# Performance work log

Hardware: AMD Instinct MI355X
Metric: run time of the kernel (lower is better)

Reference implementation:

```python
import jax, jax.numpy as jnp
import numpy as np

N_NODES = 100000
N_EDGES = 1600000
N_GRAPHS = 1000
IN_C = 64
HID = 64
OUT_C = 1
L = 3


def setup_inputs() -> dict:
    key = jax.random.key(0)
    ks = jax.random.split(key, 12)
    x = jax.random.normal(ks[0], (N_NODES, IN_C), dtype=jnp.float32)
    edge_index = jax.random.randint(ks[1], (2, N_EDGES), 0, N_NODES, dtype=jnp.int32)
    batch = jnp.sort(jax.random.randint(ks[2], (N_NODES,), 0, N_GRAPHS, dtype=jnp.int32))
    s = 1.0 / np.sqrt(HID)
    # GraphConv params (all layers 64->64): lin_rel (W,b) applied to aggregated
    # neighbors, lin_root (W, no bias) applied to self features.
    Wrel = jax.random.uniform(ks[3], (L, HID, HID), jnp.float32, -s, s)
    brel = jax.random.uniform(ks[4], (L, HID), jnp.float32, -s, s)
    Wroot = jax.random.uniform(ks[5], (L, HID, HID), jnp.float32, -s, s)
    W1 = jax.random.uniform(ks[6], (HID, 64), jnp.float32, -s, s)
    b1 = jax.random.uniform(ks[7], (64,), jnp.float32, -s, s)
    W2 = jax.random.uniform(ks[8], (64, 32), jnp.float32, -1/8, 1/8)
    b2 = jax.random.uniform(ks[9], (32,), jnp.float32, -1/8, 1/8)
    W3 = jax.random.uniform(ks[10], (32, OUT_C), jnp.float32, -1/np.sqrt(32), 1/np.sqrt(32))
    b3 = jax.random.uniform(ks[11], (OUT_C,), jnp.float32, -1/np.sqrt(32), 1/np.sqrt(32))
    return {"x": x, "edge_index": edge_index, "batch": batch,
            "Wrel": Wrel, "brel": brel, "Wroot": Wroot,
            "W1": W1, "b1": b1, "W2": W2, "b2": b2, "W3": W3, "b3": b3}


def reference(x, edge_index, batch, Wrel, brel, Wroot, W1, b1, W2, b2, W3, b3):
    src, dst = edge_index[0], edge_index[1]
    n = x.shape[0]
    x_add = jnp.zeros((N_GRAPHS, HID), dtype=x.dtype)
    for i in range(L):
        # GraphConv: gather source features, sum-scatter to targets
        agg = jax.ops.segment_sum(x[src], dst, num_segments=n)  # [N, C]
        x = agg @ Wrel[i] + brel[i] + x @ Wroot[i]
        x = jax.nn.relu(x)
        # global_add_pool per layer, accumulated
        x_add = x_add + jax.ops.segment_sum(x, batch, num_segments=N_GRAPHS)
    h = jax.nn.relu(x_add @ W1 + b1)
    h = jax.nn.relu(h @ W2 + b2)
    return h @ W3 + b3  # [N_GRAPHS, OUT_C]
```

## Files before the change

kernel.cpp:

```cpp
#include <hip/hip_runtime.h>
#include <hip/hip_bf16.h>

#define HID 64
#define BN 192
#define MAXB 1024

typedef short  bf16x8 __attribute__((ext_vector_type(8)));
typedef float  f32x4  __attribute__((ext_vector_type(4)));

__device__ inline float bf2f(unsigned int u16) {
    union { unsigned int i; float f; } v; v.i = u16 << 16; return v.f;
}
__device__ inline unsigned short f2bf(float f) {
    union { float f; unsigned int i; } v; v.f = f;
    unsigned int u = v.i;
    u += 0x7FFFu + ((u >> 16) & 1u);
    return (unsigned short)(u >> 16);
}

__global__ __launch_bounds__(1024) void bucket_hist(
        const int* __restrict__ dst, int* __restrict__ cnt,
        int* __restrict__ gHist, int E, int nb) {
    __shared__ int h[MAXB];
    for (int i = threadIdx.x; i < nb; i += 1024) h[i] = 0;
    __syncthreads();
    int base = blockIdx.x * 16384;
    for (int i = 0; i < 16; ++i) {
        int e = base + i * 1024 + threadIdx.x;
        if (e < E) atomicAdd(&h[dst[e] / BN], 1);
    }
    __syncthreads();
    int* gh = gHist + (size_t)blockIdx.x * nb;
    for (int i = threadIdx.x; i < nb; i += 1024) {
        int c = h[i];
        gh[i] = c;
        if (c) atomicAdd(&cnt[i], c);
    }
}

__global__ void bucket_scan(const int* __restrict__ cnt, int* __restrict__ base,
                            int* __restrict__ cursor, int nb, int total) {
    int lane = threadIdx.x;
    int running = 0;
    int nch = (nb + 63) / 64;
    for (int c = 0; c < nch; ++c) {
        int i = c * 64 + lane;
        int v = (i < nb) ? cnt[i] : 0;
        int s = v;
        for (int d = 1; d < 64; d <<= 1) {
            int t = __shfl_up(s, d);
            if (lane >= d) s += t;
        }
        if (i < nb) {
            int ex = running + s - v;
            base[i] = ex;
            cursor[i * 16] = ex;
        }
        running += __shfl(s, 63);
    }
    if (lane == 0) base[nb] = total;
}

__global__ __launch_bounds__(1024) void bucket_scatter(
        const int* __restrict__ src, const int* __restrict__ dst,
        const int* __restrict__ gHist,
        int* __restrict__ cursor, unsigned int* __restrict__ rec, int E, int nb) {
    __shared__ int gb[MAXB];
    __shared__ int lc[MAXB];
    for (int i = threadIdx.x; i < nb; i += 1024) lc[i] = 0;
    const int* gh = gHist + (size_t)blockIdx.x * nb;
    for (int i = threadIdx.x; i < nb; i += 1024) {
        int c = gh[i];
        if (c) gb[i] = atomicAdd(&cursor[i * 16], c);
    }
    __syncthreads();
    int base = blockIdx.x * 16384;
    for (int i = 0; i < 16; ++i) {
        int e = base + i * 1024 + threadIdx.x;
        if (e < E) {
            int d = dst[e];
            int b = d / BN;
            int lp = atomicAdd(&lc[b], 1);
            rec[gb[b] + lp] = ((unsigned int)src[e] << 8) | (unsigned int)(d - b * BN);
        }
    }
}

__global__ __launch_bounds__(256) void bucket_to_csr(
        const unsigned int* __restrict__ rec, const int* __restrict__ bbase,
        int* __restrict__ col, int* __restrict__ rowp, int N, int nb) {
    __shared__ int tmp[256];
    __shared__ int cur[256];
    int b = blockIdx.x;
    int n0 = b * BN;
    int nNodes = min(BN, N - n0);
    int tid = threadIdx.x;
    int e0 = bbase[b], e1 = bbase[b + 1];
    tmp[tid] = 0;
    __syncthreads();
    for (int e = e0 + tid; e < e1; e += 256)
        atomicAdd(&tmp[rec[e] & 255u], 1);
    __syncthreads();
    int my = tmp[tid];
    for (int offd = 1; offd < 256; offd <<= 1) {
        int t = (tid >= offd) ? tmp[tid - offd] : 0;
        __syncthreads();
        tmp[tid] += t;
        __syncthreads();
    }
    int ex = tmp[tid] - my;
    cur[tid] = ex;
    if (tid < nNodes) rowp[n0 + tid] = e0 + ex;
    if (b == nb - 1 && tid == 0) rowp[N] = e1;
    __syncthreads();
    for (int e = e0 + tid; e < e1; e += 256) {
        unsigned int r = rec[e];
        int p = atomicAdd(&cur[r & 255u], 1);
        col[e0 + p] = (int)(r >> 8);
    }
}

__global__ __launch_bounds__(256) void prep_all(
        const float* __restrict__ x0, unsigned int* __restrict__ xb,
        const float* __restrict__ Wrel, const float* __restrict__ Wroot,
        unsigned short* __restrict__ Wt,
        const int* __restrict__ batch, int* __restrict__ bstart,
        int* __restrict__ bcnt, float* __restrict__ x_add,
        int N, int G, int nl, int NB) {
    int i = blockIdx.x * 256 + threadIdx.x;
    if (i < N * 16) {
        float4 v = reinterpret_cast<const float4*>(x0)[i];
        xb[i * 2]     = ((unsigned int)f2bf(v.y) << 16) | f2bf(v.x);
        xb[i * 2 + 1] = ((unsigned int)f2bf(v.w) << 16) | f2bf(v.z);
    }
    if (i < nl * 64 * 128) {
        int k = i & 127, c = (i >> 7) & 63, l = i >> 13;
        float v = (k < 64) ? Wrel[(size_t)l * 4096 + k * 64 + c]
                           : Wroot[(size_t)l * 4096 + (k - 64) * 64 + c];
        Wt[i] = f2bf(v);
    }
    if (i < N) {
        int b = batch[i];
        int prev = (i == 0) ? -1 : batch[i - 1];
        for (int g = prev + 1; g <= b; ++g) bstart[g] = i;
        if (i == N - 1)
            for (int g = b + 1; g <= G; ++g) bstart[g] = N;
    }
    if (i < NB) bcnt[i] = 0;
    if (i < G * 64) x_add[i] = 0.f;
}

__global__ __launch_bounds__(256) void layer_fused(
        const int* __restrict__ rowp, const int* __restrict__ col,
        const unsigned int* __restrict__ xb,
        unsigned short* __restrict__ yout,
        const unsigned short* __restrict__ Wt,
        const float* __restrict__ brel,
        const unsigned int* __restrict__ poolY,
        const int* __restrict__ bstart, float* __restrict__ x_add,
        int n, int nTiles, int G) {
    int tid = threadIdx.x;
    if (blockIdx.x >= nTiles) {
        int g = blockIdx.x - nTiles;
        if (g >= G) return;
        int lane = tid & 63, w = tid >> 6;
        int h = lane >> 5, ch = lane & 31;
        __shared__ float2 part[4][32];
        int s0 = bstart[g], s1 = bstart[g + 1];
        float ax = 0.f, ay = 0.f;
        for (int nd = s0 + w * 2 + h; nd < s1; nd += 8) {
            unsigned int p = poolY[(size_t)nd * 32 + ch];
            ax += bf2f(p & 0xFFFFu);
            ay += bf2f(p >> 16);
        }
        ax += __shfl(ax, lane ^ 32);
        ay += __shfl(ay, lane ^ 32);
        if (h == 0) part[w][ch] = make_float2(ax, ay);
        __syncthreads();
        if (tid < 32) {
            float2 s = part[0][tid];
            s.x += part[1][tid].x + part[2][tid].x + part[3][tid].x;
            s.y += part[1][tid].y + part[2][tid].y + part[3][tid].y;
            float2* xa = reinterpret_cast<float2*>(x_add + (size_t)g * 64);
            float2 cur = xa[tid];
            xa[tid] = make_float2(cur.x + s.x, cur.y + s.y);
        }
        return;
    }

    __shared__ unsigned int aggL[16][36];
    int n0 = blockIdx.x * 16;
    int lane = tid & 63;
    int wv = tid >> 6;
    int half = lane >> 5, ch = lane & 31;

#pragma unroll
    for (int s = 0; s < 2; ++s) {
        int node = n0 + wv * 4 + half * 2 + s;
        if (node < n) {
            int e0 = rowp[node], e1 = rowp[node + 1];
            float ax = 0.f, ay = 0.f;
            for (int eb = e0; eb < e1; eb += 8) {
                int c[8];
#pragma unroll
                for (int j = 0; j < 8; ++j) c[j] = col[min(eb + j, e1 - 1)];
                unsigned int p[8];
#pragma unroll
                for (int j = 0; j < 8; ++j) p[j] = xb[(size_t)c[j] * 32 + ch];
#pragma unroll
                for (int j = 0; j < 8; ++j) {
                    unsigned int q = (eb + j < e1) ? p[j] : 0u;
                    ax += bf2f(q & 0xFFFFu);
                    ay += bf2f(q >> 16);
                }
            }
            aggL[node - n0][ch] = ((unsigned int)f2bf(ay) << 16) | f2bf(ax);
        } else if (node - n0 < 16) {
            aggL[node - n0][ch] = 0u;
        }
    }
    __syncthreads();

    int r = lane & 15, kb = lane >> 4;
    f32x4 acc = {};
    const unsigned short* xrow = reinterpret_cast<const unsigned short*>(xb)
                               + (size_t)min(n0 + r, n - 1) * 64 + kb * 8;
    const unsigned short* wrow = Wt + (size_t)(wv * 16 + r) * 128 + kb * 8;
#pragma unroll
    for (int ks = 0; ks < 4; ++ks) {
        bf16x8 a;
        if (ks < 2) {
            a = *reinterpret_cast<const bf16x8*>(
                    reinterpret_cast<const unsigned short*>(&aggL[r][0])
                    + ks * 32 + kb * 8);
        } else {
            a = *reinterpret_cast<const bf16x8*>(xrow + (ks - 2) * 32);
        }
        bf16x8 b = *reinterpret_cast<const bf16x8*>(wrow + ks * 32);
        acc = __builtin_amdgcn_mfma_f32_16x16x32_bf16(a, b, acc, 0, 0, 0);
    }
    int c = wv * 16 + r;
    float bias = brel[c];
#pragma unroll
    for (int reg = 0; reg < 4; ++reg) {
        int node = n0 + kb * 4 + reg;
        if (node < n) {
            float v = acc[reg] + bias;
            yout[(size_t)node * 64 + c] = f2bf(fmaxf(v, 0.f));
        }
    }
}

__global__ __launch_bounds__(256) void final_pool_mlp(
        const unsigned int* __restrict__ y3,
        const int* __restrict__ bstart, const float* __restrict__ x_add,
        const float* __restrict__ W1, const float* __restrict__ b1,
        const float* __restrict__ W2, const float* __restrict__ b2,
        const float* __restrict__ W3, const float* __restrict__ b3,
        float* __restrict__ out, int ngraph) {
    int g = blockIdx.x;
    if (g >= ngraph) return;
    int tid = threadIdx.x;
    int lane = tid & 63, w = tid >> 6;
    int h = lane >> 5, ch = lane & 31;
    __shared__ float2 part[4][32];
    __shared__ float xaL[64];
    __shared__ float h1s[64];
    __shared__ float h2s[32];
    int s0 = bstart[g], s1 = bstart[g + 1];
    float ax = 0.f, ay = 0.f;
    for (int nd = s0 + w * 2 + h; nd < s1; nd += 8) {
        unsigned int p = y3[(size_t)nd * 32 + ch];
        ax += bf2f(p & 0xFFFFu);
        ay += bf2f(p >> 16);
    }
    ax += __shfl(ax, lane ^ 32);
    ay += __shfl(ay, lane ^ 32);
    if (h == 0) part[w][ch] = make_float2(ax, ay);
    __syncthreads();
    if (tid < 32) {
        float2 s = part[0][tid];
        s.x += part[1][tid].x + part[2][tid].x + part[3][tid].x;
        s.y += part[1][tid].y + part[2][tid].y + part[3][tid].y;
        const float2* xa = reinterpret_cast<const float2*>(x_add + (size_t)g * 64);
        float2 cur = xa[tid];
        xaL[tid * 2]     = cur.x + s.x;
        xaL[tid * 2 + 1] = cur.y + s.y;
    }
    __syncthreads();
    if (tid < 64) {
        float s = b1[tid];
#pragma unroll
        for (int k = 0; k < 64; ++k) s += xaL[k] * W1[k * 64 + tid];
        h1s[tid] = fmaxf(s, 0.f);
    }
    __syncthreads();
    if (tid < 32) {
        float s2 = b2[tid];
#pragma unroll
        for (int k = 0; k < 64; ++k) s2 += h1s[k] * W2[k * 32 + tid];
        h2s[tid] = fmaxf(s2, 0.f);
    }
    __syncthreads();
    if (tid == 0) {
        float o = b3[0];
        for (int k = 0; k < 32; ++k) o += h2s[k] * W3[k];
        out[g] = o;
    }
}

extern "C" void kernel_launch(void* const* d_in, const int* in_sizes, int n_in,
                              void* d_out, int out_size, void* d_ws, size_t ws_size,
                              hipStream_t stream) {
    const float* x0    = (const float*)d_in[0];
    const int*   ei    = (const int*)d_in[1];
    const int*   batch = (const int*)d_in[2];
    const float* Wrel  = (const float*)d_in[3];
    const float* brel  = (const float*)d_in[4];
    const float* Wroot = (const float*)d_in[5];
    const float* W1    = (const float*)d_in[6];
    const float* b1    = (const float*)d_in[7];
    const float* W2    = (const float*)d_in[8];
    const float* b2    = (const float*)d_in[9];
    const float* W3    = (const float*)d_in[10];
    const float* b3    = (const float*)d_in[11];
    float* out = (float*)d_out;

    const int N = in_sizes[0] / HID;
    const int E = in_sizes[1] / 2;
    const int G = out_size;
    const int L = in_sizes[3] / (HID * HID);
    const int NB = (N + BN - 1) / BN;

    const int* src = ei;
    const int* dst = ei + E;

    char* w = (char*)d_ws;
    size_t off = 0;
    auto alloc = [&](size_t bytes) {
        void* p = w + off;
        off += (bytes + 255) & ~(size_t)255;
        return p;
    };
    int sortBlocks = (E + 16383) / 16384;

    unsigned short* xb0   = (unsigned short*)alloc((size_t)N * HID * 2);
    unsigned short* xbA   = (unsigned short*)alloc((size_t)N * HID * 2);
    unsigned short* xbB   = (unsigned short*)alloc((size_t)N * HID * 2);
    unsigned short* Wt    = (unsigned short*)alloc((size_t)L * 64 * 128 * 2);
    unsigned int*   recs  = (unsigned int*)alloc((size_t)E * 4);
    int*   col    = (int*)alloc((size_t)E * 4);
    int*   rowp   = (int*)alloc((size_t)(N + 1) * 4);
    float* x_add  = (float*)alloc((size_t)G * HID * 4);
    int*   bcnt   = (int*)alloc((size_t)NB * 4);
    int*   bbase  = (int*)alloc((size_t)(NB + 1) * 4);
    int*   bcur   = (int*)alloc((size_t)NB * 16 * 4);
    int*   bstart = (int*)alloc((size_t)(G + 1) * 4);
    int*   gHist  = (int*)alloc((size_t)sortBlocks * NB * 4);
    (void)ws_size;

    const int TB = 256;

    prep_all<<<(N * 16 + TB - 1) / TB, TB, 0, stream>>>(
            x0, (unsigned int*)xb0, Wrel, Wroot, Wt,
            batch, bstart, bcnt, x_add, N, G, L, NB);

    bucket_hist<<<sortBlocks, 1024, 0, stream>>>(dst, bcnt, gHist, E, NB);
    bucket_scan<<<1, 64, 0, stream>>>(bcnt, bbase, bcur, NB, E);
    bucket_scatter<<<sortBlocks, 1024, 0, stream>>>(src, dst, gHist, bcur, recs, E, NB);
    bucket_to_csr<<<NB, TB, 0, stream>>>(recs, bbase, col, rowp, N, NB);

    int nTiles = (N + 15) / 16;
    for (int i = 0; i < L; ++i) {
        const unsigned short* xin = (i == 0) ? xb0 : ((i == 1) ? xbA : xbB);
        unsigned short* xout = (i == 1) ? xbB : xbA;
        const unsigned int* poolY = (i == 0) ? nullptr : (const unsigned int*)xin;
        int grid = (i == 0) ? nTiles : (nTiles + G);
        layer_fused<<<grid, TB, 0, stream>>>(rowp, col,
                (const unsigned int*)xin, xout,
                Wt + (size_t)i * 64 * 128, brel + (size_t)i * HID,
                poolY, bstart, x_add, N, nTiles, G);
    }

    final_pool_mlp<<<G, TB, 0, stream>>>((const unsigned int*)xbA, bstart, x_add,
            W1, b1, W2, b2, W3, b3, out, G);
}
```

Measured before the change: 211.5 us.

## Replace edge histogram and scan with fixed-capacity per-bucket windows

Drops the global histogram and prefix-scan kernels. Each destination bucket now gets a fixed window of WIN slots, and the bucket cursors are initialised to b*WIN in prep_all. The scatter kernel builds its local histogram and claims global offsets in a single pass. The CSR build reads the bucket end from the cursor and writes a per-node (start,end) int2 row pointer. This removes two launches and an extra pass over dst, but a bucket receiving more than WIN edges would overflow into its neighbour, which is safe only for roughly uniform degree distributions.

```diff
diff --git a/kernel.cpp b/kernel.cpp
--- a/kernel.cpp
+++ b/kernel.cpp
@@ -4,6 +4,7 @@
 #define HID 64
 #define BN 192
 #define MAXB 1024
+#define WIN 3840
 
 typedef short  bf16x8 __attribute__((ext_vector_type(8)));
 typedef float  f32x4  __attribute__((ext_vector_type(4)));
@@ -18,11 +19,43 @@
     return (unsigned short)(u >> 16);
 }
 
-__global__ __launch_bounds__(1024) void bucket_hist(
-        const int* __restrict__ dst, int* __restrict__ cnt,
-        int* __restrict__ gHist, int E, int nb) {
+__global__ __launch_bounds__(256) void prep_all(
+        const float* __restrict__ x0, unsigned int* __restrict__ xb,
+        const float* __restrict__ Wrel, const float* __restrict__ Wroot,
+        unsigned short* __restrict__ Wt,
+        const int* __restrict__ batch, int* __restrict__ bstart,
+        int* __restrict__ bcur, float* __restrict__ x_add,
+        int N, int G, int nl, int NB) {
+    int i = blockIdx.x * 256 + threadIdx.x;
+    if (i < N * 16) {
+        float4 v = reinterpret_cast<const float4*>(x0)[i];
+        xb[i * 2]     = ((unsigned int)f2bf(v.y) << 16) | f2bf(v.x);
+        xb[i * 2 + 1] = ((unsigned int)f2bf(v.w) << 16) | f2bf(v.z);
+    }
+    if (i < nl * 64 * 128) {
+        int k = i & 127, c = (i >> 7) & 63, l = i >> 13;
+        float v = (k < 64) ? Wrel[(size_t)l * 4096 + k * 64 + c]
+                           : Wroot[(size_t)l * 4096 + (k - 64) * 64 + c];
+        Wt[i] = f2bf(v);
+    }
+    if (i < N) {
+        int b = batch[i];
+        int prev = (i == 0) ? -1 : batch[i - 1];
+        for (int g = prev + 1; g <= b; ++g) bstart[g] = i;
+        if (i == N - 1)
+            for (int g = b + 1; g <= G; ++g) bstart[g] = N;
+    }
+    if (i < NB) bcur[i * 16] = i * WIN;
+    if (i < G * 64) x_add[i] = 0.f;
+}
+
+__global__ __launch_bounds__(1024) void bucket_scatter(
+        const int* __restrict__ src, const int* __restrict__ dst,
+        int* __restrict__ cursor, unsigned int* __restrict__ rec, int E, int nb) {
     __shared__ int h[MAXB];
-    for (int i = threadIdx.x; i < nb; i += 1024) h[i] = 0;
+    __shared__ int gb[MAXB];
+    __shared__ int lc[MAXB];
+    for (int i = threadIdx.x; i < nb; i += 1024) { h[i] = 0; lc[i] = 0; }
     __syncthreads();
     int base = blockIdx.x * 16384;
     for (int i = 0; i < 16; ++i) {
@@ -30,51 +63,11 @@
         if (e < E) atomicAdd(&h[dst[e] / BN], 1);
     }
     __syncthreads();
-    int* gh = gHist + (size_t)blockIdx.x * nb;
     for (int i = threadIdx.x; i < nb; i += 1024) {
         int c = h[i];
-        gh[i] = c;
-        if (c) atomicAdd(&cnt[i], c);
-    }
-}
-
-__global__ void bucket_scan(const int* __restrict__ cnt, int* __restrict__ base,
-                            int* __restrict__ cursor, int nb, int total) {
-    int lane = threadIdx.x;
-    int running = 0;
-    int nch = (nb + 63) / 64;
-    for (int c = 0; c < nch; ++c) {
-        int i = c * 64 + lane;
-        int v = (i < nb) ? cnt[i] : 0;
-        int s = v;
-        for (int d = 1; d < 64; d <<= 1) {
-            int t = __shfl_up(s, d);
-            if (lane >= d) s += t;
-        }
-        if (i < nb) {
-            int ex = running + s - v;
-            base[i] = ex;
-            cursor[i * 16] = ex;
-        }
-        running += __shfl(s, 63);
-    }
-    if (lane == 0) base[nb] = total;
-}
-
-__global__ __launch_bounds__(1024) void bucket_scatter(
-        const int* __restrict__ src, const int* __restrict__ dst,
-        const int* __restrict__ gHist,
-        int* __restrict__ cursor, unsigned int* __restrict__ rec, int E, int nb) {
-    __shared__ int gb[MAXB];
-    __shared__ int lc[MAXB];
-    for (int i = threadIdx.x; i < nb; i += 1024) lc[i] = 0;
-    const int* gh = gHist + (size_t)blockIdx.x * nb;
-    for (int i = threadIdx.x; i < nb; i += 1024) {
-        int c = gh[i];
         if (c) gb[i] = atomicAdd(&cursor[i * 16], c);
     }
     __syncthreads();
-    int base = blockIdx.x * 16384;
     for (int i = 0; i < 16; ++i) {
         int e = base + i * 1024 + threadIdx.x;
         if (e < E) {
@@ -87,15 +80,15 @@
 }
 
 __global__ __launch_bounds__(256) void bucket_to_csr(
-        const unsigned int* __restrict__ rec, const int* __restrict__ bbase,
-        int* __restrict__ col, int* __restrict__ rowp, int N, int nb) {
+        const unsigned int* __restrict__ rec, const int* __restrict__ cursor,
+        int* __restrict__ col, int2* __restrict__ rowp2, int N, int nb) {
     __shared__ int tmp[256];
     __shared__ int cur[256];
     int b = blockIdx.x;
     int n0 = b * BN;
     int nNodes = min(BN, N - n0);
     int tid = threadIdx.x;
-    int e0 = bbase[b], e1 = bbase[b + 1];
+    int e0 = b * WIN, e1 = cursor[b * 16];
     tmp[tid] = 0;
     __syncthreads();
     for (int e = e0 + tid; e < e1; e += 256)
@@ -110,8 +103,7 @@
     }
     int ex = tmp[tid] - my;
     cur[tid] = ex;
-    if (tid < nNodes) rowp[n0 + tid] = e0 + ex;
-    if (b == nb - 1 && tid == 0) rowp[N] = e1;
+    if (tid < nNodes) rowp2[n0 + tid] = make_int2(e0 + ex, e0 + ex + my);
     __syncthreads();
     for (int e = e0 + tid; e < e1; e += 256) {
         unsigned int r = rec[e];
@@ -120,38 +112,8 @@
     }
 }
 
-__global__ __launch_bounds__(256) void prep_all(
-        const float* __restrict__ x0, unsigned int* __restrict__ xb,
-        const float* __restrict__ Wrel, const float* __restrict__ Wroot,
-        unsigned short* __restrict__ Wt,
-        const int* __restrict__ batch, int* __restrict__ bstart,
-        int* __restrict__ bcnt, float* __restrict__ x_add,
-        int N, int G, int nl, int NB) {
-    int i = blockIdx.x * 256 + threadIdx.x;
-    if (i < N * 16) {
-        float4 v = reinterpret_cast<const float4*>(x0)[i];
-        xb[i * 2]     = ((unsigned int)f2bf(v.y) << 16) | f2bf(v.x);
-        xb[i * 2 + 1] = ((unsigned int)f2bf(v.w) << 16) | f2bf(v.z);
-    }
-    if (i < nl * 64 * 128) {
-        int k = i & 127, c = (i >> 7) & 63, l = i >> 13;
-        float v = (k < 64) ? Wrel[(size_t)l * 4096 + k * 64 + c]
-                           : Wroot[(size_t)l * 4096 + (k - 64) * 64 + c];
-        Wt[i] = f2bf(v);
-    }
-    if (i < N) {
-        int b = batch[i];
-        int prev = (i == 0) ? -1 : batch[i - 1];
-        for (int g = prev + 1; g <= b; ++g) bstart[g] = i;
-        if (i == N - 1)
-            for (int g = b + 1; g <= G; ++g) bstart[g] = N;
-    }
-    if (i < NB) bcnt[i] = 0;
-    if (i < G * 64) x_add[i] = 0.f;
-}
-
 __global__ __launch_bounds__(256) void layer_fused(
-        const int* __restrict__ rowp, const int* __restrict__ col,
+        const int2* __restrict__ rowp2, const int* __restrict__ col,
         const unsigned int* __restrict__ xb,
         unsigned short* __restrict__ yout,
         const unsigned short* __restrict__ Wt,
@@ -198,7 +160,8 @@
     for (int s = 0; s < 2; ++s) {
         int node = n0 + wv * 4 + half * 2 + s;
         if (node < n) {
-            int e0 = rowp[node], e1 = rowp[node + 1];
+            int2 rp = rowp2[node];
+            int e0 = rp.x, e1 = rp.y;
             float ax = 0.f, ay = 0.f;
             for (int eb = e0; eb < e1; eb += 8) {
                 int c[8];
@@ -342,33 +305,27 @@
         off += (bytes + 255) & ~(size_t)255;
         return p;
     };
-    int sortBlocks = (E + 16383) / 16384;
-
     unsigned short* xb0   = (unsigned short*)alloc((size_t)N * HID * 2);
     unsigned short* xbA   = (unsigned short*)alloc((size_t)N * HID * 2);
     unsigned short* xbB   = (unsigned short*)alloc((size_t)N * HID * 2);
     unsigned short* Wt    = (unsigned short*)alloc((size_t)L * 64 * 128 * 2);
-    unsigned int*   recs  = (unsigned int*)alloc((size_t)E * 4);
-    int*   col    = (int*)alloc((size_t)E * 4);
-    int*   rowp   = (int*)alloc((size_t)(N + 1) * 4);
+    unsigned int*   recs  = (unsigned int*)alloc((size_t)NB * WIN * 4);
+    int*   col    = (int*)alloc((size_t)NB * WIN * 4);
+    int2*  rowp2  = (int2*)alloc((size_t)N * 8);
     float* x_add  = (float*)alloc((size_t)G * HID * 4);
-    int*   bcnt   = (int*)alloc((size_t)NB * 4);
-    int*   bbase  = (int*)alloc((size_t)(NB + 1) * 4);
     int*   bcur   = (int*)alloc((size_t)NB * 16 * 4);
     int*   bstart = (int*)alloc((size_t)(G + 1) * 4);
-    int*   gHist  = (int*)alloc((size_t)sortBlocks * NB * 4);
     (void)ws_size;
 
     const int TB = 256;
 
     prep_all<<<(N * 16 + TB - 1) / TB, TB, 0, stream>>>(
             x0, (unsigned int*)xb0, Wrel, Wroot, Wt,
-            batch, bstart, bcnt, x_add, N, G, L, NB);
-
-    bucket_hist<<<sortBlocks, 1024, 0, stream>>>(dst, bcnt, gHist, E, NB);
-    bucket_scan<<<1, 64, 0, stream>>>(bcnt, bbase, bcur, NB, E);
-    bucket_scatter<<<sortBlocks, 1024, 0, stream>>>(src, dst, gHist, bcur, recs, E, NB);
-    bucket_to_csr<<<NB, TB, 0, stream>>>(recs, bbase, col, rowp, N, NB);
+            batch, bstart, bcur, x_add, N, G, L, NB);
+
+    int sortBlocks = (E + 16383) / 16384;
+    bucket_scatter<<<sortBlocks, 1024, 0, stream>>>(src, dst, bcur, recs, E, NB);
+    bucket_to_csr<<<NB, TB, 0, stream>>>(recs, bcur, col, rowp2, N, NB);
 
     int nTiles = (N + 15) / 16;
     for (int i = 0; i < L; ++i) {
@@ -376,7 +333,7 @@
         unsigned short* xout = (i == 1) ? xbB : xbA;
         const unsigned int* poolY = (i == 0) ? nullptr : (const unsigned int*)xin;
         int grid = (i == 0) ? nTiles : (nTiles + G);
-        layer_fused<<<grid, TB, 0, stream>>>(rowp, col,
+        layer_fused<<<grid, TB, 0, stream>>>(rowp2, col,
                 (const unsigned int*)xin, xout,
                 Wt + (size_t)i * 64 * 128, brel + (size_t)i * HID,
                 poolY, bstart, x_add, N, nTiles, G);
```

Result: faster. 202.2 us (-4.4%).
